# Performance work log

Hardware: AMD Instinct MI355X
Metric: run time of the kernel (lower is better)

Reference implementation:

```python
import jax, jax.numpy as jnp
import numpy as np

D_MODEL = 1024
N_HEADS = 16
D_HEAD = 64
SEQ = 2048
BATCH = 2
ATTN_SCALE = float(np.sqrt(D_HEAD))  # cfg.use_attn_scale = True
NEG_INF = -1e9


def setup_inputs() -> dict:
    key = jax.random.key(0)
    ks = jax.random.split(key, 8)
    s = 0.02
    return {
        "query_input": jax.random.normal(ks[0], (BATCH, SEQ, D_MODEL), jnp.float32),
        "key_input": jax.random.normal(ks[1], (BATCH, SEQ, D_MODEL), jnp.float32),
        "value_input": jax.random.normal(ks[2], (BATCH, SEQ, D_MODEL), jnp.float32),
        "W_Q": jax.random.normal(ks[3], (N_HEADS, D_MODEL, D_HEAD), jnp.float32) * s,
        "W_K": jax.random.normal(ks[4], (N_HEADS, D_MODEL, D_HEAD), jnp.float32) * s,
        "W_V": jax.random.normal(ks[5], (N_HEADS, D_MODEL, D_HEAD), jnp.float32) * s,
        "W_O": jax.random.normal(ks[6], (N_HEADS, D_HEAD, D_MODEL), jnp.float32) * s,
        "b_Q": jnp.zeros((N_HEADS, D_HEAD), jnp.float32),
        "b_K": jnp.zeros((N_HEADS, D_HEAD), jnp.float32),
        "b_V": jnp.zeros((N_HEADS, D_HEAD), jnp.float32),
        "b_O": jnp.zeros((D_MODEL,), jnp.float32),
    }


def reference(query_input, key_input, value_input, W_Q, W_K, W_V, W_O, b_Q, b_K, b_V, b_O):
    # QKV projections: [batch, pos, d_model] x [head, d_model, d_head] -> [batch, pos, head, d_head]
    q = jnp.einsum("bpd,hde->bphe", query_input, W_Q) + b_Q
    k = jnp.einsum("bpd,hde->bphe", key_input, W_K) + b_K
    v = jnp.einsum("bpd,hde->bphe", value_input, W_V) + b_V

    # attn scores [batch, head, query_pos, key_pos]
    scores = jnp.einsum("bqhe,bkhe->bhqk", q, k) / ATTN_SCALE

    # causal mask (attn_type == 'global'): tril over [n_ctx, n_ctx] sliced to seq
    causal = jnp.tril(jnp.ones((SEQ, SEQ), bool))
    scores = jnp.where(causal[None, None, :, :], scores, NEG_INF)

    pattern = jax.nn.softmax(scores, axis=-1)

    # z: [batch, query_pos, head, d_head]
    z = jnp.einsum("bhqk,bkhe->bqhe", pattern, v)

    # output projection: [batch, pos, d_model]
    out = jnp.einsum("bqhe,hed->bqd", z, W_O) + b_O
    return out
```

## Files before the change

### kernel.cpp

```cpp
#include <hip/hip_runtime.h>
#include <stdint.h>


typedef __attribute__((ext_vector_type(8))) short short8;
typedef __attribute__((ext_vector_type(4))) short short4v;
typedef __attribute__((ext_vector_type(4))) float floatx4;
typedef __attribute__((ext_vector_type(4))) unsigned int uintx4;
typedef __attribute__((ext_vector_type(2))) unsigned int uint2v;

#define MFMA16(a, b, c) __builtin_amdgcn_mfma_f32_16x16x32_bf16(a, b, c, 0, 0, 0)

#if __has_builtin(__builtin_amdgcn_mfma_f32_16x16x16bf16_1k)
#define HAVE_K16 1
#define MFMAK16(a, b, c) __builtin_amdgcn_mfma_f32_16x16x16bf16_1k(a, b, c, 0, 0, 0)
#else
#define HAVE_K16 0
#endif

__device__ __forceinline__ unsigned short f2b(float f) {
  unsigned int u = __builtin_bit_cast(unsigned int, f);
  u = (u + 0x7fffu + ((u >> 16) & 1u)) >> 16;
  return (unsigned short)u;
}
__device__ __forceinline__ float exp2f_fast(float x) {
#if __has_builtin(__builtin_amdgcn_exp2f)
  return __builtin_amdgcn_exp2f(x);
#else
  return exp2f(x);
#endif
}
__device__ __forceinline__ unsigned int pack2_bf16(float lo, float hi) {
#if __has_builtin(__builtin_amdgcn_perm)
  return __builtin_amdgcn_perm(__builtin_bit_cast(unsigned int, hi),
                               __builtin_bit_cast(unsigned int, lo), 0x07060302u);
#else
  return (__builtin_bit_cast(unsigned int, lo) >> 16) |
         (__builtin_bit_cast(unsigned int, hi) & 0xffff0000u);
#endif
}

__device__ __forceinline__ void async_copy16(void* lds, const void* g) {
  __builtin_amdgcn_global_load_lds(
      (const __attribute__((address_space(1))) unsigned int*)g,
      (__attribute__((address_space(3))) unsigned int*)lds, 16, 0, 0);
}

__device__ __forceinline__ void xpose4(floatx4& v, int lane) {
  {
    float s0 = __shfl_xor(v[1], 1, 64);
    float s1 = __shfl_xor(v[0], 1, 64);
    float s2 = __shfl_xor(v[3], 1, 64);
    float s3 = __shfl_xor(v[2], 1, 64);
    if (lane & 1) { v[0] = s0; v[2] = s2; } else { v[1] = s1; v[3] = s3; }
  }
  {
    float s0 = __shfl_xor(v[2], 2, 64);
    float s1 = __shfl_xor(v[3], 2, 64);
    float s2 = __shfl_xor(v[0], 2, 64);
    float s3 = __shfl_xor(v[1], 2, 64);
    if (lane & 2) { v[0] = s0; v[1] = s1; } else { v[2] = s2; v[3] = s3; }
  }
}

__global__ __launch_bounds__(256) void convall(
    const float* __restrict__ Xq, const float* __restrict__ Xk,
    const float* __restrict__ Xv, const float* __restrict__ WQ,
    const float* __restrict__ WK, const float* __restrict__ WV,
    const float* __restrict__ WO, unsigned short* __restrict__ xout,
    unsigned short* __restrict__ wout, unsigned short* __restrict__ woout) {
  __shared__ float T[64][65];
  const int bid = blockIdx.x;
  const int t = threadIdx.x;
  if (bid < 12288) {
    const int yy = bid / 4096, x = bid - yy * 4096;
    const float* in = (yy == 0) ? Xq : ((yy == 1) ? Xk : Xv);
    size_t i = (size_t)x * 256 + t;
    float4 v = ((const float4*)in)[i];
    ushort4 u;
    u.x = f2b(v.x); u.y = f2b(v.y); u.z = f2b(v.z); u.w = f2b(v.w);
    ((ushort4*)(xout + (size_t)yy * 4194304))[i] = u;
    return;
  }
  const int rr = t >> 4, cc = t & 15;
  if (bid < 13056) {
    const int sub = bid - 12288;
    const int yy = sub >> 8, x = sub & 255;
    const float* in = (yy == 0) ? WQ : ((yy == 1) ? WK : WV);
    const int h = x >> 4, d0 = (x & 15) << 6;
#pragma unroll
    for (int it = 0; it < 4; ++it) {
      int dl = it * 16 + rr;
      float4 v = *(const float4*)&in[(size_t)h * 65536 + (size_t)(d0 + dl) * 64 + cc * 4];
      T[dl][cc * 4 + 0] = v.x; T[dl][cc * 4 + 1] = v.y;
      T[dl][cc * 4 + 2] = v.z; T[dl][cc * 4 + 3] = v.w;
    }
    __syncthreads();
    unsigned short* ob = wout + (size_t)yy * 1048576;
#pragma unroll
    for (int it = 0; it < 4; ++it) {
      int e = it * 16 + rr;
      ushort4 u;
      u.x = f2b(T[cc * 4 + 0][e]); u.y = f2b(T[cc * 4 + 1][e]);
      u.z = f2b(T[cc * 4 + 2][e]); u.w = f2b(T[cc * 4 + 3][e]);
      *(ushort4*)&ob[(size_t)(h * 64 + e) * 1024 + d0 + cc * 4] = u;
    }
    return;
  }
  {
    const int x = bid - 13056;
    const int r0 = (x & 15) << 6, c0 = (x >> 4) << 6;
#pragma unroll
    for (int it = 0; it < 4; ++it) {
      int rl = it * 16 + rr;
      float4 v = *(const float4*)&WO[(size_t)(r0 + rl) * 1024 + c0 + cc * 4];
      T[rl][cc * 4 + 0] = v.x; T[rl][cc * 4 + 1] = v.y;
      T[rl][cc * 4 + 2] = v.z; T[rl][cc * 4 + 3] = v.w;
    }
    __syncthreads();
#pragma unroll
    for (int it = 0; it < 4; ++it) {
      int dl = it * 16 + rr;
      ushort4 u;
      u.x = f2b(T[cc * 4 + 0][dl]); u.y = f2b(T[cc * 4 + 1][dl]);
      u.z = f2b(T[cc * 4 + 2][dl]); u.w = f2b(T[cc * 4 + 3][dl]);
      *(ushort4*)&woout[(size_t)(c0 + dl) * 1024 + r0 + cc * 4] = u;
    }
  }
}

template <int TM, int TN, int NZ>
__global__ __launch_bounds__(512, (TM == 128) ? 6 : 4) void gemm512(
    const short* __restrict__ A0, const short* __restrict__ A1,
    const short* __restrict__ A2, const short* __restrict__ B0,
    const short* __restrict__ B1, const short* __restrict__ B2,
    const float* __restrict__ bias0, const float* __restrict__ bias1,
    const float* __restrict__ bias2, unsigned short* __restrict__ ob0,
    unsigned short* __restrict__ ob1, unsigned short* __restrict__ ob2,
    float* __restrict__ outf, float qscale) {
  constexpr int WAVES_N = (TN == 128) ? 2 : 4;
  constexpr int NJ = TN / (WAVES_N * 16);
  constexpr int NY = 4096 / TM;
  __shared__ short As[TM * 64];
  __shared__ short Bs[TN * 64];

  const int L = blockIdx.x;
  const int x = L / (NY * NZ);
  const int r = L - x * (NY * NZ);
  const int y = r / NZ;
  const int z = r - y * NZ;

  const short* A = (z == 0) ? A0 : (z == 1) ? A1 : A2;
  const short* Bt = (z == 0) ? B0 : (z == 1) ? B1 : B2;

  const int tid = threadIdx.x;
  const int lane = tid & 63, w = tid >> 6;
  const int quad = lane >> 4, col = lane & 15;
  const int m0 = y * TM, n0 = x * TN;
  const int wm = (w / WAVES_N) * 32, wn = (w % WAVES_N) * (NJ * 16);

  floatx4 acc[2][NJ] = {};

  const int slr = lane >> 3, sgc = (lane & 7) ^ slr;
  const short* ga = A + (size_t)(m0 + w * (TM / 8) + slr) * 1024 + sgc * 8;
  const short* gb = Bt + (size_t)(n0 + w * (TN / 8) + slr) * 1024 + sgc * 8;
  const int fsw = col & 7;

  for (int k0 = 0; k0 < 1024; k0 += 64) {
    if (TM == 128) {
      async_copy16(&As[(w * 16) * 64], ga);
      async_copy16(&As[(w * 16 + 8) * 64], ga + 8 * 1024);
    } else {
      async_copy16(&As[(w * 8) * 64], ga);
    }
    if (TN == 128) {
      async_copy16(&Bs[(w * 16) * 64], gb);
      async_copy16(&Bs[(w * 16 + 8) * 64], gb + 8 * 1024);
    } else {
      async_copy16(&Bs[(w * 8) * 64], gb);
    }
    ga += 64; gb += 64;
    __syncthreads();
#pragma unroll
    for (int kk = 0; kk < 2; ++kk) {
      short8 af[2], bf[NJ];
#pragma unroll
      for (int mi = 0; mi < 2; ++mi)
        af[mi] = *(const short8*)&As[(wm + mi * 16 + col) * 64 +
                                     (((kk * 4 + quad) ^ fsw) * 8)];
#pragma unroll
      for (int nj = 0; nj < NJ; ++nj)
        bf[nj] = *(const short8*)&Bs[(wn + nj * 16 + col) * 64 +
                                     (((kk * 4 + quad) ^ fsw) * 8)];
#pragma unroll
      for (int mi = 0; mi < 2; ++mi)
#pragma unroll
        for (int nj = 0; nj < NJ; ++nj)
          acc[mi][nj] = MFMA16(af[mi], bf[nj], acc[mi][nj]);
    }
    __syncthreads();
  }

  const float* bias = (z == 0) ? bias0 : (z == 1) ? bias1 : bias2;
  unsigned short* outb = (z == 0) ? ob0 : (z == 1) ? ob1 : ob2;
  const int mode = (NZ == 3) ? ((z == 2) ? 2 : 1) : 0;
  const float scale = (NZ == 3 && z == 0) ? qscale : 1.0f;

  float bv[NJ];
#pragma unroll
  for (int nj = 0; nj < NJ; ++nj) bv[nj] = bias[n0 + wn + nj * 16 + col];

  if (mode == 2) {
#pragma unroll
    for (int mi = 0; mi < 2; ++mi)
#pragma unroll
      for (int nj = 0; nj < NJ; ++nj) {
        int m = m0 + wm + mi * 16 + quad * 4;
        int n = n0 + wn + nj * 16 + col;
        int bb = m >> 11, s = m & 2047, h = n >> 6, e = n & 63;
        ushort4 u;
        u.x = f2b(acc[mi][nj][0] + bv[nj]);
        u.y = f2b(acc[mi][nj][1] + bv[nj]);
        u.z = f2b(acc[mi][nj][2] + bv[nj]);
        u.w = f2b(acc[mi][nj][3] + bv[nj]);
        *(ushort4*)&outb[(((size_t)bb * 16 + h) * 64 + e) * 2048 + s] = u;
      }
  } else {
#pragma unroll
    for (int mi = 0; mi < 2; ++mi)
#pragma unroll
      for (int nj = 0; nj < NJ; ++nj) {
        floatx4 v;
#pragma unroll
        for (int rr = 0; rr < 4; ++rr) v[rr] = (acc[mi][nj][rr] + bv[nj]) * scale;
        xpose4(v, lane);
        int m = m0 + wm + mi * 16 + quad * 4 + (col & 3);
        int nb = n0 + wn + nj * 16 + (col & ~3);
        if (mode == 0) {
          *(floatx4*)&outf[(size_t)m * 1024 + nb] = v;
        } else {
          int bb = m >> 11, s = m & 2047, h = nb >> 6, e = nb & 63;
          ushort4 u;
          u.x = f2b(v[0]); u.y = f2b(v[1]); u.z = f2b(v[2]); u.w = f2b(v[3]);
          *(ushort4*)&outb[(((size_t)bb * 16 + h) * 2048 + s) * 64 + e] = u;
        }
      }
  }
}

#if !HAVE_K16
__device__ __forceinline__ void exchange4(const unsigned int* u01,
                                          const unsigned int* u23, int srcA,
                                          int srcB, bool hiq, short8& pf0,
                                          short8& pf1) {
  unsigned int xA0 = (unsigned int)__shfl((int)u01[0], srcA, 64);
  unsigned int xA1 = (unsigned int)__shfl((int)u01[1], srcA, 64);
  unsigned int yA0 = (unsigned int)__shfl((int)u23[0], srcA, 64);
  unsigned int yA1 = (unsigned int)__shfl((int)u23[1], srcA, 64);
  unsigned int xB0 = (unsigned int)__shfl((int)u01[0], srcB, 64);
  unsigned int xB1 = (unsigned int)__shfl((int)u01[1], srcB, 64);
  unsigned int yB0 = (unsigned int)__shfl((int)u23[0], srcB, 64);
  unsigned int yB1 = (unsigned int)__shfl((int)u23[1], srcB, 64);
  uintx4 v0;
  v0.x = hiq ? xA1 : xA0; v0.y = hiq ? yA1 : yA0;
  v0.z = hiq ? xB1 : xB0; v0.w = hiq ? yB1 : yB0;
  pf0 = __builtin_bit_cast(short8, v0);
  xA0 = (unsigned int)__shfl((int)u01[2], srcA, 64);
  xA1 = (unsigned int)__shfl((int)u01[3], srcA, 64);
  yA0 = (unsigned int)__shfl((int)u23[2], srcA, 64);
  yA1 = (unsigned int)__shfl((int)u23[3], srcA, 64);
  xB0 = (unsigned int)__shfl((int)u01[2], srcB, 64);
  xB1 = (unsigned int)__shfl((int)u01[3], srcB, 64);
  yB0 = (unsigned int)__shfl((int)u23[2], srcB, 64);
  yB1 = (unsigned int)__shfl((int)u23[3], srcB, 64);
  uintx4 v1;
  v1.x = hiq ? xA1 : xA0; v1.y = hiq ? yA1 : yA0;
  v1.z = hiq ? xB1 : xB0; v1.w = hiq ? yB1 : yB0;
  pf1 = __builtin_bit_cast(short8, v1);
}
#endif

__device__ __forceinline__ void stage_kv(short* Kbuf, short* Vbuf,
                                         const short* kg, const short* vg,
                                         int kv0, int w, int slr, int sgc) {
  const short* kr = kg + (size_t)(kv0 + w * 16 + slr) * 64 + sgc * 8;
  async_copy16(&Kbuf[(w * 16) * 64], kr);
  async_copy16(&Kbuf[(w * 16 + 8) * 64], kr + 8 * 64);
  const short* vr = vg + (size_t)(w * 16 + slr) * 2048 + kv0 + sgc * 8;
  async_copy16(&Vbuf[(w * 16) * 64], vr);
  async_copy16(&Vbuf[(w * 16 + 8) * 64], vr + 8 * 2048);
}

__global__ __launch_bounds__(256) void attn(const short* __restrict__ q,
                                            const short* __restrict__ k,
                                            const short* __restrict__ vt,
                                            unsigned short* __restrict__ z) {
  __shared__ short Ks[2][64 * 64];
  __shared__ short Vs[2][64 * 64];

  const int tid = threadIdx.x;
  const int lane = tid & 63, w = tid >> 6;
  const int quad = lane >> 4, col = lane & 15;
  const int qt = 31 - (blockIdx.x >> 5), bh = blockIdx.x & 31;
  const int q0 = qt * 64, qw0 = q0 + w * 16;
  const size_t base = (size_t)bh * (2048 * 64);

  const short* qp = q + base + (size_t)(qw0 + col) * 64 + quad * 8;
  short8 bq0 = *(const short8*)qp;
  short8 bq1 = *(const short8*)(qp + 32);

  floatx4 o[4] = {};
  float m_run = -1e30f, l_run = 0.f;

  const short* kg = k + base;
  const short* vg = vt + base;
  const int ksw = col & 7;
  const int slr = lane >> 3, sgc = (lane & 7) ^ slr;
#if !HAVE_K16
  const int srcA = ((quad & 1) << 5) + col, srcB = srcA + 16;
  const bool hiq = (quad & 2) != 0;
#endif

  stage_kv(Ks[0], Vs[0], kg, vg, 0, w, slr, sgc);
  int p = 0;

  for (int t = 0; t <= qt; ++t) {
    __syncthreads();
    if (t < qt) stage_kv(Ks[p ^ 1], Vs[p ^ 1], kg, vg, (t + 1) * 64, w, slr, sgc);

    const bool diag = (t == qt);
    const int mtmax = diag ? w : 3;

    floatx4 st[4];
#pragma unroll
    for (int mt = 0; mt < 4; ++mt) {
      if (mt <= mtmax) {
        const short* kb = &Ks[p][(mt * 16 + col) * 64];
        short8 ka0 = *(const short8*)(kb + (quad ^ ksw) * 8);
        short8 ka1 = *(const short8*)(kb + ((quad + 4) ^ ksw) * 8);
        floatx4 a = {0.f, 0.f, 0.f, 0.f};
        a = MFMA16(ka0, bq0, a);
        a = MFMA16(ka1, bq1, a);
        if (diag && mt == mtmax) {
#pragma unroll
          for (int r = 0; r < 4; ++r)
            if (quad * 4 + r > col) a[r] = -1e9f;
        }
        st[mt] = a;
      }
    }

    float pmax = -3e38f;
#pragma unroll
    for (int mt = 0; mt < 4; ++mt)
      if (mt <= mtmax) {
#pragma unroll
        for (int r = 0; r < 4; ++r) pmax = fmaxf(pmax, st[mt][r]);
      }
    pmax = fmaxf(pmax, __shfl_xor(pmax, 16, 64));
    pmax = fmaxf(pmax, __shfl_xor(pmax, 32, 64));
    float mnew = fmaxf(m_run, pmax);
    float alpha = exp2f_fast(m_run - mnew);
    m_run = mnew;

    unsigned int u01[4], u23[4];
    float lsum = 0.f;
#pragma unroll
    for (int mt = 0; mt < 4; ++mt) {
      if (mt <= mtmax) {
        float p0 = exp2f_fast(st[mt][0] - mnew);
        float p1 = exp2f_fast(st[mt][1] - mnew);
        float p2 = exp2f_fast(st[mt][2] - mnew);
        float p3 = exp2f_fast(st[mt][3] - mnew);
        lsum += (p0 + p1) + (p2 + p3);
        u01[mt] = pack2_bf16(p0, p1);
        u23[mt] = pack2_bf16(p2, p3);
      } else {
        u01[mt] = 0u; u23[mt] = 0u;
      }
    }
    lsum += __shfl_xor(lsum, 16, 64);
    lsum += __shfl_xor(lsum, 32, 64);
    l_run = l_run * alpha + lsum;

#if HAVE_K16
    short4v pb[4];
#pragma unroll
    for (int mt = 0; mt < 4; ++mt) {
      uint2v uu;
      uu.x = u01[mt]; uu.y = u23[mt];
      pb[mt] = __builtin_bit_cast(short4v, uu);
    }
#pragma unroll
    for (int et = 0; et < 4; ++et) {
      const short* vrow = &Vs[p][(et * 16 + col) * 64];
      floatx4 t0 = o[et];
#pragma unroll
      for (int r = 0; r < 4; ++r) t0[r] *= alpha;
#pragma unroll
      for (int mt = 0; mt < 4; ++mt) {
        if (mt <= mtmax) {
          int c = mt * 2 + (quad >> 1);
          short4v va = *(const short4v*)&vrow[((c ^ ksw) * 8) + (quad & 1) * 4];
          t0 = MFMAK16(va, pb[mt], t0);
        }
      }
      o[et] = t0;
    }
#else
    short8 pf0, pf1;
    exchange4(u01, u23, srcA, srcB, hiq, pf0, pf1);
#pragma unroll
    for (int et = 0; et < 4; ++et) {
      const short* vb = &Vs[p][(et * 16 + col) * 64];
      short8 va0 = *(const short8*)(vb + (quad ^ ksw) * 8);
      short8 va1 = *(const short8*)(vb + ((quad + 4) ^ ksw) * 8);
      floatx4 t0 = o[et];
#pragma unroll
      for (int r = 0; r < 4; ++r) t0[r] *= alpha;
      t0 = MFMA16(va0, pf0, t0);
      t0 = MFMA16(va1, pf1, t0);
      o[et] = t0;
    }
#endif
    p ^= 1;
  }

  const int b = bh >> 4, h = bh & 15;
#if __has_builtin(__builtin_amdgcn_rcpf)
  const float invl = __builtin_amdgcn_rcpf(l_run);
#else
  const float invl = 1.f / l_run;
#endif
  unsigned short* zr = z + (((size_t)b * 2048 + qw0 + col) * 16 + h) * 64;
#pragma unroll
  for (int et = 0; et < 4; ++et) {
    ushort4 u;
    u.x = f2b(o[et][0] * invl); u.y = f2b(o[et][1] * invl);
    u.z = f2b(o[et][2] * invl); u.w = f2b(o[et][3] * invl);
    *(ushort4*)&zr[et * 16 + quad * 4] = u;
  }
}

extern "C" void kernel_launch(void* const* d_in, const int* in_sizes, int n_in,
                              void* d_out, int out_size, void* d_ws, size_t ws_size,
                              hipStream_t stream) {
  (void)in_sizes; (void)n_in; (void)out_size; (void)ws_size;
  const float* Xq = (const float*)d_in[0];
  const float* Xk = (const float*)d_in[1];
  const float* Xv = (const float*)d_in[2];
  const float* WQ = (const float*)d_in[3];
  const float* WK = (const float*)d_in[4];
  const float* WV = (const float*)d_in[5];
  const float* WO = (const float*)d_in[6];
  const float* bQ = (const float*)d_in[7];
  const float* bK = (const float*)d_in[8];
  const float* bV = (const float*)d_in[9];
  const float* bO = (const float*)d_in[10];
  float* out = (float*)d_out;

  unsigned short* xqb = (unsigned short*)d_ws;
  unsigned short* xkb = xqb + 4194304;
  unsigned short* xvb = xkb + 4194304;
  unsigned short* wqt = xvb + 4194304;
  unsigned short* wkt = wqt + 1048576;
  unsigned short* wvt = wkt + 1048576;
  unsigned short* wot = wvt + 1048576;
  unsigned short* qb = wot + 1048576;
  unsigned short* kb = qb + 4194304;
  unsigned short* vtb = kb + 4194304;
  unsigned short* zb = vtb + 4194304;

  convall<<<13312, 256, 0, stream>>>(Xq, Xk, Xv, WQ, WK, WV, WO, xqb, wqt, wot);

  const float qscale = 0.125f * 1.44269504088896f;
  gemm512<128, 128, 3><<<768, 512, 0, stream>>>(
      (const short*)xqb, (const short*)xkb, (const short*)xvb,
      (const short*)wqt, (const short*)wkt, (const short*)wvt, bQ, bK, bV, qb,
      kb, vtb, nullptr, qscale);

  attn<<<1024, 256, 0, stream>>>((const short*)qb, (const short*)kb,
                                 (const short*)vtb, zb);

  gemm512<64, 64, 1><<<1024, 512, 0, stream>>>(
      (const short*)zb, (const short*)zb, (const short*)zb, (const short*)wot,
      (const short*)wot, (const short*)wot, bO, bO, bO, nullptr, nullptr,
      nullptr, out, 1.0f);
}
```

Baseline: 219.0 us.

## Fuse fp32-to-bf16 activation conversion into QKV projection GEMM A-tile loads

```diff
diff --git a/kernel.cpp b/kernel.cpp
--- a/kernel.cpp
+++ b/kernel.cpp
@@ -21,6 +21,9 @@
   unsigned int u = __builtin_bit_cast(unsigned int, f);
   u = (u + 0x7fffu + ((u >> 16) & 1u)) >> 16;
   return (unsigned short)u;
+}
+__device__ __forceinline__ unsigned int packf2b(float lo, float hi) {
+  return (unsigned int)f2b(lo) | ((unsigned int)f2b(hi) << 16);
 }
 __device__ __forceinline__ float exp2f_fast(float x) {
 #if __has_builtin(__builtin_amdgcn_exp2f)
@@ -62,29 +65,16 @@
   }
 }
 
-__global__ __launch_bounds__(256) void convall(
-    const float* __restrict__ Xq, const float* __restrict__ Xk,
-    const float* __restrict__ Xv, const float* __restrict__ WQ,
-    const float* __restrict__ WK, const float* __restrict__ WV,
-    const float* __restrict__ WO, unsigned short* __restrict__ xout,
+__global__ __launch_bounds__(256) void convw(
+    const float* __restrict__ WQ, const float* __restrict__ WK,
+    const float* __restrict__ WV, const float* __restrict__ WO,
     unsigned short* __restrict__ wout, unsigned short* __restrict__ woout) {
   __shared__ float T[64][65];
   const int bid = blockIdx.x;
   const int t = threadIdx.x;
-  if (bid < 12288) {
-    const int yy = bid / 4096, x = bid - yy * 4096;
-    const float* in = (yy == 0) ? Xq : ((yy == 1) ? Xk : Xv);
-    size_t i = (size_t)x * 256 + t;
-    float4 v = ((const float4*)in)[i];
-    ushort4 u;
-    u.x = f2b(v.x); u.y = f2b(v.y); u.z = f2b(v.z); u.w = f2b(v.w);
-    ((ushort4*)(xout + (size_t)yy * 4194304))[i] = u;
-    return;
-  }
   const int rr = t >> 4, cc = t & 15;
-  if (bid < 13056) {
-    const int sub = bid - 12288;
-    const int yy = sub >> 8, x = sub & 255;
+  if (bid < 768) {
+    const int yy = bid >> 8, x = bid & 255;
     const float* in = (yy == 0) ? WQ : ((yy == 1) ? WK : WV);
     const int h = x >> 4, d0 = (x & 15) << 6;
 #pragma unroll
@@ -107,7 +97,7 @@
     return;
   }
   {
-    const int x = bid - 13056;
+    const int x = bid - 768;
     const int r0 = (x & 15) << 6, c0 = (x >> 4) << 6;
 #pragma unroll
     for (int it = 0; it < 4; ++it) {
@@ -128,7 +118,7 @@
   }
 }
 
-template <int TM, int TN, int NZ>
+template <int TM, int TN, int NZ, int CONVA>
 __global__ __launch_bounds__(512, (TM == 128) ? 6 : 4) void gemm512(
     const short* __restrict__ A0, const short* __restrict__ A1,
     const short* __restrict__ A2, const short* __restrict__ B0,
@@ -160,17 +150,46 @@
 
   floatx4 acc[2][NJ] = {};
 
-  const int slr = lane >> 3, sgc = (lane & 7) ^ slr;
+  const int slr = lane >> 3, sch = lane & 7;
+  const int sgc = sch ^ slr;
   const short* ga = A + (size_t)(m0 + w * (TM / 8) + slr) * 1024 + sgc * 8;
   const short* gb = Bt + (size_t)(n0 + w * (TN / 8) + slr) * 1024 + sgc * 8;
   const int fsw = col & 7;
 
+  const float* gaf0 = nullptr;
+  const float* gaf1 = nullptr;
+  uintx4* awp0 = nullptr;
+  uintx4* awp1 = nullptr;
+  float4 a00, a01, a10, a11;
+  if (CONVA) {
+    const float* Af = (const float*)A;
+    gaf0 = Af + (size_t)(m0 + w * 16 + slr) * 1024 + sgc * 8;
+    gaf1 = gaf0 + 8 * 1024;
+    awp0 = (uintx4*)&As[(w * 16 + slr) * 64 + sch * 8];
+    awp1 = (uintx4*)&As[(w * 16 + 8 + slr) * 64 + sch * 8];
+    a00 = *(const float4*)gaf0;
+    a01 = *(const float4*)(gaf0 + 4);
+    a10 = *(const float4*)gaf1;
+    a11 = *(const float4*)(gaf1 + 4);
+  }
+
   for (int k0 = 0; k0 < 1024; k0 += 64) {
-    if (TM == 128) {
-      async_copy16(&As[(w * 16) * 64], ga);
-      async_copy16(&As[(w * 16 + 8) * 64], ga + 8 * 1024);
+    if (CONVA) {
+      uintx4 p0, p1;
+      p0.x = packf2b(a00.x, a00.y); p0.y = packf2b(a00.z, a00.w);
+      p0.z = packf2b(a01.x, a01.y); p0.w = packf2b(a01.z, a01.w);
+      p1.x = packf2b(a10.x, a10.y); p1.y = packf2b(a10.z, a10.w);
+      p1.z = packf2b(a11.x, a11.y); p1.w = packf2b(a11.z, a11.w);
+      *awp0 = p0;
+      *awp1 = p1;
     } else {
-      async_copy16(&As[(w * 8) * 64], ga);
+      if (TM == 128) {
+        async_copy16(&As[(w * 16) * 64], ga);
+        async_copy16(&As[(w * 16 + 8) * 64], ga + 8 * 1024);
+      } else {
+        async_copy16(&As[(w * 8) * 64], ga);
+      }
+      ga += 64;
     }
     if (TN == 128) {
       async_copy16(&Bs[(w * 16) * 64], gb);
@@ -178,7 +197,14 @@
     } else {
       async_copy16(&Bs[(w * 8) * 64], gb);
     }
-    ga += 64; gb += 64;
+    gb += 64;
+    if (CONVA && k0 < 960) {
+      gaf0 += 64; gaf1 += 64;
+      a00 = *(const float4*)gaf0;
+      a01 = *(const float4*)(gaf0 + 4);
+      a10 = *(const float4*)gaf1;
+      a11 = *(const float4*)(gaf1 + 4);
+    }
     __syncthreads();
 #pragma unroll
     for (int kk = 0; kk < 2; ++kk) {
@@ -458,10 +484,7 @@
   const float* bO = (const float*)d_in[10];
   float* out = (float*)d_out;
 
-  unsigned short* xqb = (unsigned short*)d_ws;
-  unsigned short* xkb = xqb + 4194304;
-  unsigned short* xvb = xkb + 4194304;
-  unsigned short* wqt = xvb + 4194304;
+  unsigned short* wqt = (unsigned short*)d_ws;
   unsigned short* wkt = wqt + 1048576;
   unsigned short* wvt = wkt + 1048576;
   unsigned short* wot = wvt + 1048576;
@@ -470,18 +493,18 @@
   unsigned short* vtb = kb + 4194304;
   unsigned short* zb = vtb + 4194304;
 
-  convall<<<13312, 256, 0, stream>>>(Xq, Xk, Xv, WQ, WK, WV, WO, xqb, wqt, wot);
+  convw<<<1024, 256, 0, stream>>>(WQ, WK, WV, WO, wqt, wot);
 
   const float qscale = 0.125f * 1.44269504088896f;
-  gemm512<128, 128, 3><<<768, 512, 0, stream>>>(
-      (const short*)xqb, (const short*)xkb, (const short*)xvb,
+  gemm512<128, 128, 3, 1><<<768, 512, 0, stream>>>(
+      (const short*)Xq, (const short*)Xk, (const short*)Xv,
       (const short*)wqt, (const short*)wkt, (const short*)wvt, bQ, bK, bV, qb,
       kb, vtb, nullptr, qscale);
 
   attn<<<1024, 256, 0, stream>>>((const short*)qb, (const short*)kb,
                                  (const short*)vtb, zb);
 
-  gemm512<64, 64, 1><<<1024, 512, 0, stream>>>(
+  gemm512<64, 64, 1, 0><<<1024, 512, 0, stream>>>(
       (const short*)zb, (const short*)zb, (const short*)zb, (const short*)wot,
       (const short*)wot, (const short*)wot, bO, bO, bO, nullptr, nullptr,
       nullptr, out, 1.0f);
```

After: 221.4 us. Within noise of the previous version (+1.1%).
